# Kernel optimization log

Measured on AMD Instinct MI355X. Metric: run time of the kernel, lower is better.

The kernel has to match this reference:

```python
import jax, jax.numpy as jnp
import numpy as np

VOCAB = 32000
EMBED = 8      # == d_k == n_qubits (forced by the module's reshapes)
NQ = 8
DEPTH = 2
NBLOCKS = 6
FFN = 8        # == n_qubits (forced)
NCLASSES = 10
B, S = 32, 1024
LN_EPS = 1e-5

_H = np.array([[1.0, 1.0], [1.0, -1.0]], np.complex64) / np.sqrt(2.0).astype(np.float32)


def _posenc(seq, dim):
    pos = np.arange(seq, dtype=np.float32)[:, None]
    div = np.exp(np.arange(0, dim, 2, dtype=np.float32) * (-np.log(10000.0) / dim))
    pe = np.zeros((seq, dim), np.float32)
    pe[:, 0::2] = np.sin(pos * div)
    pe[:, 1::2] = np.cos(pos * div)
    return jnp.asarray(pe)


def _quantum_head(x, depth=DEPTH):
    """Batched statevector simulation of the QNode. x: (N, NQ) angles -> (N, NQ) Z expvals."""
    N, n = x.shape
    c = jnp.cos(0.5 * x).astype(jnp.complex64)
    s = jnp.sin(0.5 * x).astype(jnp.complex64)
    amp = jnp.stack([c, -1j * s], axis=-1)  # (N, n, 2): RX(theta)|0>
    state = amp[:, 0]  # product state built wire by wire -> (N, 2, ..., 2)
    for i in range(1, n):
        state = state[..., None] * amp[:, i].reshape((N,) + (1,) * (state.ndim - 1) + (2,))
    Hm = jnp.asarray(_H)
    for _ in range(depth):
        for i in range(n - 1):  # CNOT(i, i+1): flip target slice where control==1
            s0 = jnp.take(state, 0, axis=i + 1)
            s1 = jnp.flip(jnp.take(state, 1, axis=i + 1), axis=i + 1)
            state = jnp.stack([s0, s1], axis=i + 1)
        state = jnp.einsum('...i,ij->...j', state, Hm)  # Hadamard on last wire
    probs = state.real ** 2 + state.imag ** 2  # (N, 2, ..., 2)
    zs = []
    for i in range(n):
        axes = tuple(a for a in range(1, n + 1) if a != i + 1)
        m = probs.sum(axis=axes)  # (N, 2) marginal of wire i
        zs.append(m[:, 0] - m[:, 1])
    return jnp.stack(zs, axis=-1)


def _ln(x, g, b):
    m = x.mean(axis=-1, keepdims=True)
    v = ((x - m) ** 2).mean(axis=-1, keepdims=True)
    return g * (x - m) / jnp.sqrt(v + LN_EPS) + b


def _forward(tokens, emb, ln1_g, ln1_b, ln2_g, ln2_b, attn_w, attn_b,
             ffn_w1, ffn_b1, ffn_w2, ffn_b2, cls_w, cls_b):
    Bt, St = tokens.shape
    E = emb.shape[1]
    x = emb[tokens] + _posenc(St, E)[None]  # (B, S, E)
    scale = float(1.0 / np.sqrt(E))
    for l in range(NBLOCKS):
        # quantum attention (num_heads == 1, d_k == E)
        qkv = _quantum_head(x.reshape(-1, E)).reshape(Bt, St, E)
        scores = jnp.einsum('bqd,bkd->bqk', qkv, qkv) * scale
        attn = jax.nn.softmax(scores, axis=-1)
        out = jnp.einsum('bqk,bkd->bqd', attn, qkv)
        attn_out = out @ attn_w[l] + attn_b[l]
        x = _ln(x + attn_out, ln1_g[l], ln1_b[l])
        # quantum FFN
        h = x @ ffn_w1[l] + ffn_b1[l]  # (B, S, FFN)
        qf = _quantum_head(h.reshape(-1, FFN)).reshape(Bt, St, FFN)
        ffn_out = qf @ ffn_w2[l] + ffn_b2[l]
        x = _ln(x + ffn_out, ln2_g[l], ln2_b[l])
    pooled = x.mean(axis=1)  # (B, E)
    return pooled @ cls_w + cls_b  # (B, NCLASSES)


def setup_inputs() -> dict:
    key = jax.random.key(0)
    ks = jax.random.split(key, 8)
    f32 = jnp.float32
    L, E, F = NBLOCKS, EMBED, FFN
    return {
        'tokens': jax.random.randint(ks[0], (B, S), 0, VOCAB),
        'emb': jax.random.normal(ks[1], (VOCAB, E), f32) * 0.1,
        'ln1_g': jnp.ones((L, E), f32), 'ln1_b': jnp.zeros((L, E), f32),
        'ln2_g': jnp.ones((L, E), f32), 'ln2_b': jnp.zeros((L, E), f32),
        'attn_w': jax.random.normal(ks[2], (L, E, E), f32) * 0.3,
        'attn_b': jnp.zeros((L, E), f32),
        'ffn_w1': jax.random.normal(ks[3], (L, E, F), f32) * 0.3,
        'ffn_b1': jnp.zeros((L, F), f32),
        'ffn_w2': jax.random.normal(ks[4], (L, F, E), f32) * 0.3,
        'ffn_b2': jnp.zeros((L, E), f32),
        'cls_w': jax.random.normal(ks[5], (E, NCLASSES), f32) * 0.3,
        'cls_b': jnp.zeros((NCLASSES,), f32),
    }


def reference(tokens, emb, ln1_g, ln1_b, ln2_g, ln2_b, attn_w, attn_b,
              ffn_w1, ffn_b1, ffn_w2, ffn_b2, cls_w, cls_b):
    return _forward(tokens, emb, ln1_g, ln1_b, ln2_g, ln2_b, attn_w, attn_b,
                    ffn_w1, ffn_b1, ffn_w2, ffn_b2, cls_w, cls_b)
```

## Files before the change

kernel.cpp:

```cpp
#include <hip/hip_runtime.h>
#include <math.h>

#define EMB 8
#define SEQ 1024
#define NBATCH 32
#define NROWS (NBATCH * SEQ)
#define LNEPS 1e-5f
#define F2(l, b, c) (((l) * 32 + (b)) * 32 + (c))

typedef __attribute__((ext_vector_type(4))) unsigned u32x4;
typedef __attribute__((ext_vector_type(8))) _Float16 f16x8;
typedef __attribute__((ext_vector_type(16))) float f32x16;

union FragU { unsigned u[4]; f16x8 s; };

__device__ __forceinline__ unsigned pkrtz(float a, float b) {
    unsigned r;
    asm("v_cvt_pkrtz_f16_f32 %0, %1, %2" : "=v"(r) : "v"(a), "v"(b));
    return r;
}
__device__ __forceinline__ unsigned pk_mul_f16(unsigned a, unsigned b) {
    unsigned r;
    asm("v_pk_mul_f16 %0, %1, %2" : "=v"(r) : "v"(a), "v"(b));
    return r;
}
__device__ __forceinline__ float hw_exp2(float x) {
    return __builtin_amdgcn_exp2f(x);
}

__device__ __forceinline__ void llc_load_2rows(const unsigned short* p,
                                               u32x4* d0, u32x4* d1) {
    asm volatile(
        "global_load_dwordx4 %0, %[a], off sc0 sc1\n\t"
        "global_load_dwordx4 %1, %[a], off offset:16 sc0 sc1\n\t"
        "s_waitcnt vmcnt(0)"
        : "=&v"(*d0), "=&v"(*d1) : [a] "v"(p) : "memory");
}
__device__ __forceinline__ void llc_store_row16(unsigned short* p, u32x4 v) {
    asm volatile("global_store_dwordx4 %[a], %[x], off sc0 sc1"
                 :: [a] "v"(p), [x] "v"(v) : "memory");
}
__device__ __forceinline__ void sys_store(float* p, float v) {
    asm volatile("global_store_dword %0, %1, off sc0 sc1" :: "v"(p), "v"(v) : "memory");
}
__device__ __forceinline__ float sys_load(const float* p) {
    float r;
    asm volatile("global_load_dword %0, %1, off sc0 sc1\n\ts_waitcnt vmcnt(0)"
                 : "=v"(r) : "v"(p) : "memory");
    return r;
}
__device__ __forceinline__ unsigned sys_load_u32(const unsigned* p) {
    unsigned r;
    asm volatile("global_load_dword %0, %1, off sc0 sc1\n\ts_waitcnt vmcnt(0)"
                 : "=v"(r) : "v"(p) : "memory");
    return r;
}
__device__ __forceinline__ void sys_store_u32(unsigned* p, unsigned v) {
    asm volatile("global_store_dword %0, %1, off sc0 sc1" :: "v"(p), "v"(v) : "memory");
}

__device__ __forceinline__ void qhead(const float xv[8], float z[8]) {
    float c[8];
#pragma unroll
    for (int j = 0; j < 8; ++j) c[j] = __cosf(xv[j]);
    float e0 = c[0];
    float o1 = c[1];
    float e2 = e0 * c[2];
    float o3 = o1 * c[3];
    float e4 = e2 * c[4];
    float o5 = o3 * c[5];
    float e6 = e4 * c[6];
    z[0] = e0; z[1] = o1; z[2] = e2; z[3] = o3;
    z[4] = e4; z[5] = o5; z[6] = e6;
    z[7] = e6 * o5 * c[7];
}

__device__ __forceinline__ void embed_row(const int* __restrict__ tokens,
                                          const float* __restrict__ emb,
                                          long grow, int srow, float xv[8]) {
    int tok = tokens[grow];
    const float* e = emb + (long)tok * EMB;
    float p = (float)srow;
    xv[0] = e[0] + sinf(p);
    xv[1] = e[1] + cosf(p);
    xv[2] = e[2] + sinf(p * 0.1f);
    xv[3] = e[3] + cosf(p * 0.1f);
    xv[4] = e[4] + sinf(p * 0.01f);
    xv[5] = e[5] + cosf(p * 0.01f);
    xv[6] = e[6] + sinf(p * 0.001f);
    xv[7] = e[7] + cosf(p * 0.001f);
}

__global__ __launch_bounds__(1024) void zero_flags(unsigned* __restrict__ f) {
    for (int i = threadIdx.x; i < 6656; i += 1024) f[i] = 0u;
}

__global__ __launch_bounds__(512, 4) void qt_fused(
    const int* __restrict__ tokens, const float* __restrict__ emb,
    const float* __restrict__ attn_w, const float* __restrict__ attn_b,
    const float* __restrict__ ln1_g, const float* __restrict__ ln1_b,
    const float* __restrict__ ffn_w1, const float* __restrict__ ffn_b1,
    const float* __restrict__ ffn_w2, const float* __restrict__ ffn_b2,
    const float* __restrict__ ln2_g, const float* __restrict__ ln2_b,
    const float* __restrict__ cls_w, const float* __restrict__ cls_b,
    unsigned short* __restrict__ qkv0, unsigned short* __restrict__ qkv1,
    unsigned* __restrict__ flags, unsigned* __restrict__ pcnt,
    float* __restrict__ partial, float* __restrict__ out)
{
    __shared__ __align__(16) uint2 KbP[2][1024];
    __shared__ __align__(16) unsigned short VtH[8][1032];
    __shared__ float Olds[8][32][9];
    __shared__ float x_lds[2][32][8];
    __shared__ int isL[2];

    const int bid = blockIdx.x;
    const int group = bid & 15;
    const int chunk = bid >> 4;
    const int tid = threadIdx.x;

    const int w = tid >> 6;
    const int lane = tid & 63;
    const int ln = lane & 31;
    const int h = lane >> 5;
    const int qbase = chunk * 32;
    const unsigned B2PK = pkrtz(0.51006972f, 0.51006972f);

    for (int l = 0; l < 6; ++l) {
        const unsigned short* qr = (l & 1) ? qkv1 : qkv0;
        unsigned short* qw = (l & 1) ? qkv0 : qkv1;
        for (int ph = 0; ph < 2; ++ph) {
            const int bb = group * 2 + ph;
            {
                u32x4 d0, d1;
                if (l == 0) {
                    float e0[8], e1[8], z0[8], z1[8];
                    embed_row(tokens, emb, (long)bb * SEQ + 2 * tid, 2 * tid, e0);
                    embed_row(tokens, emb, (long)bb * SEQ + 2 * tid + 1, 2 * tid + 1, e1);
                    if ((tid >> 4) == chunk) {
                        const int lr = 2 * tid - chunk * 32;
#pragma unroll
                        for (int j = 0; j < 8; ++j) {
                            x_lds[ph][lr][j] = e0[j];
                            x_lds[ph][lr + 1][j] = e1[j];
                        }
                    }
                    qhead(e0, z0); qhead(e1, z1);
                    d0[0] = pkrtz(z0[0], z0[1]); d0[1] = pkrtz(z0[2], z0[3]);
                    d0[2] = pkrtz(z0[4], z0[5]); d0[3] = pkrtz(z0[6], z0[7]);
                    d1[0] = pkrtz(z1[0], z1[1]); d1[1] = pkrtz(z1[2], z1[3]);
                    d1[2] = pkrtz(z1[4], z1[5]); d1[3] = pkrtz(z1[6], z1[7]);
                } else {
                    const unsigned* fp = &flags[F2(l, bb, tid >> 4)];
                    while (sys_load_u32(fp) == 0u) __builtin_amdgcn_s_sleep(1);
                    llc_load_2rows(qr + ((long)bb * SEQ + 2 * tid) * 8, &d0, &d1);
                }
                u32x4 kp0, kp1;
                kp0[0] = d0[0]; kp0[1] = d0[1]; kp0[2] = d1[0]; kp0[3] = d1[1];
                kp1[0] = d0[2]; kp1[1] = d0[3]; kp1[2] = d1[2]; kp1[3] = d1[3];
                *(u32x4*)&KbP[0][2 * tid] = kp0;
                *(u32x4*)&KbP[1][2 * tid] = kp1;
#pragma unroll
                for (int c = 0; c < 8; ++c) {
                    unsigned wa = d0[c >> 1], wb = d1[c >> 1];
                    unsigned v = (c & 1) ? ((wa >> 16) | (wb & 0xFFFF0000u))
                                         : ((wa & 0xFFFFu) | (wb << 16));
                    *(unsigned*)&VtH[c][2 * tid] = v;
                }
            }
            __syncthreads();

            FragU qfB;
            {
                uint2 qh = KbP[h][qbase + ln];
                unsigned qx = pk_mul_f16(qh.x, B2PK);
                unsigned qy = pk_mul_f16(qh.y, B2PK);
                qfB.u[0] = qx; qfB.u[1] = qy; qfB.u[2] = qx; qfB.u[3] = qy;
            }
            f32x16 zc;
#pragma unroll
            for (int i = 0; i < 16; ++i) zc[i] = 0.f;
            f32x16 accA = zc, accB = zc;

#pragma unroll
            for (int t = 0; t < 4; ++t) {
                const int kbase = (w * 4 + t) * 32;
                FragU kfA;
                {
                    uint2 kh = KbP[h][kbase + ln];
                    kfA.u[0] = kh.x; kfA.u[1] = kh.y; kfA.u[2] = 0; kfA.u[3] = 0;
                }
                f32x16 s = __builtin_amdgcn_mfma_f32_32x32x16_f16(kfA.s, qfB.s, zc, 0, 0, 0);
                float p[16];
#pragma unroll
                for (int g = 0; g < 16; ++g) p[g] = hw_exp2(s[g]);

                FragU a1, a2;
#pragma unroll
                for (int vi = 0; vi < 4; ++vi) {
                    a1.u[vi] = pkrtz(p[2 * vi], p[2 * vi + 1]);
                    a2.u[vi] = pkrtz(p[8 + 2 * vi], p[8 + 2 * vi + 1]);
                }
                FragU v1h, v2h;
                if (ln < 8) {
                    const unsigned* q0 = (const unsigned*)&VtH[ln][kbase + 4 * h];
                    const unsigned* q1 = (const unsigned*)&VtH[ln][kbase + 8 + 4 * h];
                    const unsigned* q2 = (const unsigned*)&VtH[ln][kbase + 16 + 4 * h];
                    const unsigned* q3 = (const unsigned*)&VtH[ln][kbase + 24 + 4 * h];
                    v1h.u[0] = q0[0]; v1h.u[1] = q0[1]; v1h.u[2] = q1[0]; v1h.u[3] = q1[1];
                    v2h.u[0] = q2[0]; v2h.u[1] = q2[1]; v2h.u[2] = q3[0]; v2h.u[3] = q3[1];
                } else if (ln == 8) {
#pragma unroll
                    for (int i = 0; i < 4; ++i) { v1h.u[i] = 0x3C003C00u; v2h.u[i] = 0x3C003C00u; }
                } else {
#pragma unroll
                    for (int i = 0; i < 4; ++i) { v1h.u[i] = 0; v2h.u[i] = 0; }
                }
                accA = __builtin_amdgcn_mfma_f32_32x32x16_f16(a1.s, v1h.s, accA, 0, 0, 0);
                accB = __builtin_amdgcn_mfma_f32_32x32x16_f16(a2.s, v2h.s, accB, 0, 0, 0);
            }

            if (ln <= 8) {
#pragma unroll
                for (int g = 0; g < 16; ++g)
                    Olds[w][(g & 3) + 8 * (g >> 2) + 4 * h][ln] = accA[g] + accB[g];
            }
            __syncthreads();

            if ((tid >> 6) == ph && lane < 32) {
                const int r = lane;
                float o[9];
#pragma unroll
                for (int c = 0; c < 9; ++c) {
                    float s01 = Olds[0][r][c] + Olds[1][r][c];
                    float s23 = Olds[2][r][c] + Olds[3][r][c];
                    float s45 = Olds[4][r][c] + Olds[5][r][c];
                    float s67 = Olds[6][r][c] + Olds[7][r][c];
                    o[c] = (s01 + s23) + (s45 + s67);
                }
                float inv = 1.0f / o[8];
                float outv[8];
#pragma unroll
                for (int c = 0; c < 8; ++c) outv[c] = o[c] * inv;

                const float* W  = attn_w + l * 64; const float* Wb  = attn_b + l * 8;
                const float* g1 = ln1_g + l * 8;   const float* b1v = ln1_b + l * 8;
                const float* W1 = ffn_w1 + l * 64; const float* c1  = ffn_b1 + l * 8;
                const float* W2 = ffn_w2 + l * 64; const float* c2  = ffn_b2 + l * 8;
                const float* g2 = ln2_g + l * 8;   const float* b2v = ln2_b + l * 8;

                float xv[8];
#pragma unroll
                for (int j = 0; j < 8; ++j) xv[j] = x_lds[ph][r][j];

                float y[8]; float m = 0.f;
#pragma unroll
                for (int j = 0; j < 8; ++j) {
                    float vv = Wb[j];
#pragma unroll
                    for (int i = 0; i < 8; ++i) vv += outv[i] * W[i * 8 + j];
                    y[j] = xv[j] + vv;
                    m += y[j];
                }
                m *= 0.125f;
                float var = 0.f;
#pragma unroll
                for (int j = 0; j < 8; ++j) { float dd = y[j] - m; var += dd * dd; }
                var *= 0.125f;
                float rsg = rsqrtf(var + LNEPS);
                float xn[8];
#pragma unroll
                for (int j = 0; j < 8; ++j) xn[j] = g1[j] * (y[j] - m) * rsg + b1v[j];

                float hh[8];
#pragma unroll
                for (int j = 0; j < 8; ++j) {
                    float vv = c1[j];
#pragma unroll
                    for (int i = 0; i < 8; ++i) vv += xn[i] * W1[i * 8 + j];
                    hh[j] = vv;
                }
                float qff[8]; qhead(hh, qff);
                float m2 = 0.f;
#pragma unroll
                for (int j = 0; j < 8; ++j) {
                    float vv = c2[j];
#pragma unroll
                    for (int i = 0; i < 8; ++i) vv += qff[i] * W2[i * 8 + j];
                    y[j] = xn[j] + vv;
                    m2 += y[j];
                }
                m2 *= 0.125f;
                float var2 = 0.f;
#pragma unroll
                for (int j = 0; j < 8; ++j) { float dd = y[j] - m2; var2 += dd * dd; }
                var2 *= 0.125f;
                float rs2 = rsqrtf(var2 + LNEPS);
#pragma unroll
                for (int j = 0; j < 8; ++j) {
                    float xo = g2[j] * (y[j] - m2) * rs2 + b2v[j];
                    x_lds[ph][r][j] = xo;
                    xv[j] = xo;
                }

                if (l < 5) {
                    float z[8]; qhead(xv, z);
                    u32x4 pz;
                    pz[0] = pkrtz(z[0], z[1]); pz[1] = pkrtz(z[2], z[3]);
                    pz[2] = pkrtz(z[4], z[5]); pz[3] = pkrtz(z[6], z[7]);
                    llc_store_row16(qw + ((long)bb * SEQ + chunk * 32 + r) * 8, pz);
                    asm volatile("s_waitcnt vmcnt(0)" ::: "memory");
                    if (r == 0) sys_store_u32(&flags[F2(l + 1, bb, chunk)], 1u);
                }
            }
        }
    }

    if ((tid >> 6) < 2) {
        const int ph = tid >> 6;
        const int r = tid & 63;
        const int bb = group * 2 + ph;
        float a[8];
#pragma unroll
        for (int j = 0; j < 8; ++j) {
            a[j] = (r < 32) ? x_lds[ph][r][j] : 0.f;
#pragma unroll
            for (int off = 1; off <= 32; off <<= 1) a[j] += __shfl_xor(a[j], off);
        }
        if (r < 8) sys_store(&partial[(bb * 32 + chunk) * 8 + r], a[r]);
    }
    asm volatile("s_waitcnt vmcnt(0)" ::: "memory");
    __syncthreads();
    if (tid == 0) {
        unsigned r = __hip_atomic_fetch_add(&pcnt[(group * 2) * 16], 1u,
                                            __ATOMIC_RELAXED, __HIP_MEMORY_SCOPE_AGENT);
        isL[0] = (r == 31u);
    }
    if (tid == 64) {
        unsigned r = __hip_atomic_fetch_add(&pcnt[(group * 2 + 1) * 16], 1u,
                                            __ATOMIC_RELAXED, __HIP_MEMORY_SCOPE_AGENT);
        isL[1] = (r == 31u);
    }
    __syncthreads();
    if ((tid >> 6) < 2) {
        const int ph = tid >> 6;
        if (isL[ph]) {
            const int bb = group * 2 + ph;
            const int lr = tid & 63;
            int g = lr >> 3, j = lr & 7;
            float s = sys_load(&partial[(bb * 32 + g) * 8 + j])
                    + sys_load(&partial[(bb * 32 + g + 8) * 8 + j])
                    + sys_load(&partial[(bb * 32 + g + 16) * 8 + j])
                    + sys_load(&partial[(bb * 32 + g + 24) * 8 + j]);
            s += __shfl_xor(s, 8); s += __shfl_xor(s, 16); s += __shfl_xor(s, 32);
            float poolj = s * (1.0f / 1024.0f);
            int c = lr < 10 ? lr : 9;
            float o = cls_b[c];
#pragma unroll
            for (int j2 = 0; j2 < 8; ++j2)
                o += __shfl(poolj, j2) * cls_w[j2 * 10 + c];
            if (lr < 10) out[bb * 10 + lr] = o;
        }
    }
}

extern "C" void kernel_launch(void* const* d_in, const int* in_sizes, int n_in,
                              void* d_out, int out_size, void* d_ws, size_t ws_size,
                              hipStream_t stream) {
    const int*   tokens = (const int*)d_in[0];
    const float* emb    = (const float*)d_in[1];
    const float* ln1_g  = (const float*)d_in[2];
    const float* ln1_b  = (const float*)d_in[3];
    const float* ln2_g  = (const float*)d_in[4];
    const float* ln2_b  = (const float*)d_in[5];
    const float* attn_w = (const float*)d_in[6];
    const float* attn_b = (const float*)d_in[7];
    const float* ffn_w1 = (const float*)d_in[8];
    const float* ffn_b1 = (const float*)d_in[9];
    const float* ffn_w2 = (const float*)d_in[10];
    const float* ffn_b2 = (const float*)d_in[11];
    const float* cls_w  = (const float*)d_in[12];
    const float* cls_b  = (const float*)d_in[13];

    unsigned*       flags   = (unsigned*)d_ws;
    unsigned*       pcnt    = flags + 6144;
    float*          partial = (float*)(pcnt + 512);
    unsigned short* qkv0    = (unsigned short*)(partial + 8192);
    unsigned short* qkv1    = qkv0 + (long)NROWS * 8;
    float*          outp    = (float*)d_out;

    zero_flags<<<1, 1024, 0, stream>>>(flags);
    qt_fused<<<512, 512, 0, stream>>>(
        tokens, emb, attn_w, attn_b, ln1_g, ln1_b,
        ffn_w1, ffn_b1, ffn_w2, ffn_b2, ln2_g, ln2_b,
        cls_w, cls_b, qkv0, qkv1, flags, pcnt, partial, outp);
}
```

Measured before the change: 89.07 us.

## Halve grid to 256 blocks, each handling 64 query rows across two tiles

Each block now processes 64 query rows per batch (two 32-row tiles split across wave groups) instead of 32, so the grid shrinks from 512 to 256 blocks. This halves the redundant per-block work of loading and staging the full K/V sequence into shared memory and the number of cross-block flag waits. The trade is more attention work per wave (8 key tiles instead of 4) and fewer resident blocks, which may lengthen the serial per-layer critical path. Flags, partials and the final reduction are resized to match.

```diff
diff --git a/kernel.cpp b/kernel.cpp
--- a/kernel.cpp
+++ b/kernel.cpp
@@ -6,7 +6,7 @@
 #define NBATCH 32
 #define NROWS (NBATCH * SEQ)
 #define LNEPS 1e-5f
-#define F2(l, b, c) (((l) * 32 + (b)) * 32 + (c))
+#define F(l, b, c) (((l) * 32 + (b)) * 16 + (c))
 
 typedef __attribute__((ext_vector_type(4))) unsigned u32x4;
 typedef __attribute__((ext_vector_type(8))) _Float16 f16x8;
@@ -92,10 +92,10 @@
 }
 
 __global__ __launch_bounds__(1024) void zero_flags(unsigned* __restrict__ f) {
-    for (int i = threadIdx.x; i < 6656; i += 1024) f[i] = 0u;
-}
-
-__global__ __launch_bounds__(512, 4) void qt_fused(
+    for (int i = threadIdx.x; i < 3584; i += 1024) f[i] = 0u;
+}
+
+__global__ __launch_bounds__(512, 2) void qt_fused(
     const int* __restrict__ tokens, const float* __restrict__ emb,
     const float* __restrict__ attn_w, const float* __restrict__ attn_b,
     const float* __restrict__ ln1_g, const float* __restrict__ ln1_b,
@@ -110,7 +110,7 @@
     __shared__ __align__(16) uint2 KbP[2][1024];
     __shared__ __align__(16) unsigned short VtH[8][1032];
     __shared__ float Olds[8][32][9];
-    __shared__ float x_lds[2][32][8];
+    __shared__ float x_lds[2][64][8];
     __shared__ int isL[2];
 
     const int bid = blockIdx.x;
@@ -122,7 +122,9 @@
     const int lane = tid & 63;
     const int ln = lane & 31;
     const int h = lane >> 5;
-    const int qbase = chunk * 32;
+    const int qtile = w >> 2;
+    const int qu = w & 3;
+    const int r0 = tid * 2;
     const unsigned B2PK = pkrtz(0.51006972f, 0.51006972f);
 
     for (int l = 0; l < 6; ++l) {
@@ -134,10 +136,10 @@
                 u32x4 d0, d1;
                 if (l == 0) {
                     float e0[8], e1[8], z0[8], z1[8];
-                    embed_row(tokens, emb, (long)bb * SEQ + 2 * tid, 2 * tid, e0);
-                    embed_row(tokens, emb, (long)bb * SEQ + 2 * tid + 1, 2 * tid + 1, e1);
-                    if ((tid >> 4) == chunk) {
-                        const int lr = 2 * tid - chunk * 32;
+                    embed_row(tokens, emb, (long)bb * SEQ + r0, r0, e0);
+                    embed_row(tokens, emb, (long)bb * SEQ + r0 + 1, r0 + 1, e1);
+                    if ((r0 >> 6) == chunk) {
+                        const int lr = r0 - chunk * 64;
 #pragma unroll
                         for (int j = 0; j < 8; ++j) {
                             x_lds[ph][lr][j] = e0[j];
@@ -150,25 +152,26 @@
                     d1[0] = pkrtz(z1[0], z1[1]); d1[1] = pkrtz(z1[2], z1[3]);
                     d1[2] = pkrtz(z1[4], z1[5]); d1[3] = pkrtz(z1[6], z1[7]);
                 } else {
-                    const unsigned* fp = &flags[F2(l, bb, tid >> 4)];
+                    const unsigned* fp = &flags[F(l, bb, r0 >> 6)];
                     while (sys_load_u32(fp) == 0u) __builtin_amdgcn_s_sleep(1);
-                    llc_load_2rows(qr + ((long)bb * SEQ + 2 * tid) * 8, &d0, &d1);
+                    llc_load_2rows(qr + ((long)bb * SEQ + r0) * 8, &d0, &d1);
                 }
                 u32x4 kp0, kp1;
                 kp0[0] = d0[0]; kp0[1] = d0[1]; kp0[2] = d1[0]; kp0[3] = d1[1];
                 kp1[0] = d0[2]; kp1[1] = d0[3]; kp1[2] = d1[2]; kp1[3] = d1[3];
-                *(u32x4*)&KbP[0][2 * tid] = kp0;
-                *(u32x4*)&KbP[1][2 * tid] = kp1;
+                *(u32x4*)&KbP[0][r0] = kp0;
+                *(u32x4*)&KbP[1][r0] = kp1;
 #pragma unroll
                 for (int c = 0; c < 8; ++c) {
                     unsigned wa = d0[c >> 1], wb = d1[c >> 1];
                     unsigned v = (c & 1) ? ((wa >> 16) | (wb & 0xFFFF0000u))
                                          : ((wa & 0xFFFFu) | (wb << 16));
-                    *(unsigned*)&VtH[c][2 * tid] = v;
+                    *(unsigned*)&VtH[c][r0] = v;
                 }
             }
             __syncthreads();
 
+            const int qbase = chunk * 64 + qtile * 32;
             FragU qfB;
             {
                 uint2 qh = KbP[h][qbase + ln];
@@ -180,10 +183,16 @@
 #pragma unroll
             for (int i = 0; i < 16; ++i) zc[i] = 0.f;
             f32x16 accA = zc, accB = zc;
-
-#pragma unroll
-            for (int t = 0; t < 4; ++t) {
-                const int kbase = (w * 4 + t) * 32;
+            FragU v1c, v2c;
+            {
+                const unsigned fill = (ln == 8) ? 0x3C003C00u : 0u;
+#pragma unroll
+                for (int i = 0; i < 4; ++i) { v1c.u[i] = fill; v2c.u[i] = fill; }
+            }
+
+#pragma unroll 2
+            for (int t = 0; t < 8; ++t) {
+                const int kbase = ((qu << 3) | t) << 5;
                 FragU kfA;
                 {
                     uint2 kh = KbP[h][kbase + ln];
@@ -200,7 +209,7 @@
                     a1.u[vi] = pkrtz(p[2 * vi], p[2 * vi + 1]);
                     a2.u[vi] = pkrtz(p[8 + 2 * vi], p[8 + 2 * vi + 1]);
                 }
-                FragU v1h, v2h;
+                FragU v1h = v1c, v2h = v2c;
                 if (ln < 8) {
                     const unsigned* q0 = (const unsigned*)&VtH[ln][kbase + 4 * h];
                     const unsigned* q1 = (const unsigned*)&VtH[ln][kbase + 8 + 4 * h];
@@ -208,12 +217,6 @@
                     const unsigned* q3 = (const unsigned*)&VtH[ln][kbase + 24 + 4 * h];
                     v1h.u[0] = q0[0]; v1h.u[1] = q0[1]; v1h.u[2] = q1[0]; v1h.u[3] = q1[1];
                     v2h.u[0] = q2[0]; v2h.u[1] = q2[1]; v2h.u[2] = q3[0]; v2h.u[3] = q3[1];
-                } else if (ln == 8) {
-#pragma unroll
-                    for (int i = 0; i < 4; ++i) { v1h.u[i] = 0x3C003C00u; v2h.u[i] = 0x3C003C00u; }
-                } else {
-#pragma unroll
-                    for (int i = 0; i < 4; ++i) { v1h.u[i] = 0; v2h.u[i] = 0; }
                 }
                 accA = __builtin_amdgcn_mfma_f32_32x32x16_f16(a1.s, v1h.s, accA, 0, 0, 0);
                 accB = __builtin_amdgcn_mfma_f32_32x32x16_f16(a2.s, v2h.s, accB, 0, 0, 0);
@@ -226,17 +229,15 @@
             }
             __syncthreads();
 
-            if ((tid >> 6) == ph && lane < 32) {
-                const int r = lane;
+            if ((tid >> 6) == ph) {
+                const int r = tid & 63;
+                const int rr = r & 31;
+                const int w0 = (r >> 5) * 4;
                 float o[9];
 #pragma unroll
-                for (int c = 0; c < 9; ++c) {
-                    float s01 = Olds[0][r][c] + Olds[1][r][c];
-                    float s23 = Olds[2][r][c] + Olds[3][r][c];
-                    float s45 = Olds[4][r][c] + Olds[5][r][c];
-                    float s67 = Olds[6][r][c] + Olds[7][r][c];
-                    o[c] = (s01 + s23) + (s45 + s67);
-                }
+                for (int c = 0; c < 9; ++c)
+                    o[c] = (Olds[w0][rr][c] + Olds[w0 + 1][rr][c])
+                         + (Olds[w0 + 2][rr][c] + Olds[w0 + 3][rr][c]);
                 float inv = 1.0f / o[8];
                 float outv[8];
 #pragma unroll
@@ -307,9 +308,9 @@
                     u32x4 pz;
                     pz[0] = pkrtz(z[0], z[1]); pz[1] = pkrtz(z[2], z[3]);
                     pz[2] = pkrtz(z[4], z[5]); pz[3] = pkrtz(z[6], z[7]);
-                    llc_store_row16(qw + ((long)bb * SEQ + chunk * 32 + r) * 8, pz);
+                    llc_store_row16(qw + ((long)bb * SEQ + chunk * 64 + r) * 8, pz);
                     asm volatile("s_waitcnt vmcnt(0)" ::: "memory");
-                    if (r == 0) sys_store_u32(&flags[F2(l + 1, bb, chunk)], 1u);
+                    if (r == 0) sys_store_u32(&flags[F(l + 1, bb, chunk)], 1u);
                 }
             }
         }
@@ -322,23 +323,23 @@
         float a[8];
 #pragma unroll
         for (int j = 0; j < 8; ++j) {
-            a[j] = (r < 32) ? x_lds[ph][r][j] : 0.f;
+            a[j] = x_lds[ph][r][j];
 #pragma unroll
             for (int off = 1; off <= 32; off <<= 1) a[j] += __shfl_xor(a[j], off);
         }
-        if (r < 8) sys_store(&partial[(bb * 32 + chunk) * 8 + r], a[r]);
+        if (r < 8) sys_store(&partial[(bb * 16 + chunk) * 8 + r], a[r]);
     }
     asm volatile("s_waitcnt vmcnt(0)" ::: "memory");
     __syncthreads();
     if (tid == 0) {
         unsigned r = __hip_atomic_fetch_add(&pcnt[(group * 2) * 16], 1u,
                                             __ATOMIC_RELAXED, __HIP_MEMORY_SCOPE_AGENT);
-        isL[0] = (r == 31u);
+        isL[0] = (r == 15u);
     }
     if (tid == 64) {
         unsigned r = __hip_atomic_fetch_add(&pcnt[(group * 2 + 1) * 16], 1u,
                                             __ATOMIC_RELAXED, __HIP_MEMORY_SCOPE_AGENT);
-        isL[1] = (r == 31u);
+        isL[1] = (r == 15u);
     }
     __syncthreads();
     if ((tid >> 6) < 2) {
@@ -347,10 +348,8 @@
             const int bb = group * 2 + ph;
             const int lr = tid & 63;
             int g = lr >> 3, j = lr & 7;
-            float s = sys_load(&partial[(bb * 32 + g) * 8 + j])
-                    + sys_load(&partial[(bb * 32 + g + 8) * 8 + j])
-                    + sys_load(&partial[(bb * 32 + g + 16) * 8 + j])
-                    + sys_load(&partial[(bb * 32 + g + 24) * 8 + j]);
+            float s = sys_load(&partial[(bb * 16 + g) * 8 + j])
+                    + sys_load(&partial[(bb * 16 + g + 8) * 8 + j]);
             s += __shfl_xor(s, 8); s += __shfl_xor(s, 16); s += __shfl_xor(s, 32);
             float poolj = s * (1.0f / 1024.0f);
             int c = lr < 10 ? lr : 9;
@@ -382,14 +381,14 @@
     const float* cls_b  = (const float*)d_in[13];
 
     unsigned*       flags   = (unsigned*)d_ws;
-    unsigned*       pcnt    = flags + 6144;
+    unsigned*       pcnt    = flags + 3072;
     float*          partial = (float*)(pcnt + 512);
-    unsigned short* qkv0    = (unsigned short*)(partial + 8192);
+    unsigned short* qkv0    = (unsigned short*)(partial + 4096);
     unsigned short* qkv1    = qkv0 + (long)NROWS * 8;
     float*          outp    = (float*)d_out;
 
     zero_flags<<<1, 1024, 0, stream>>>(flags);
-    qt_fused<<<512, 512, 0, stream>>>(
+    qt_fused<<<256, 512, 0, stream>>>(
         tokens, emb, attn_w, attn_b, ln1_g, ln1_b,
         ffn_w1, ffn_b1, ffn_w2, ffn_b2, ln2_g, ln2_b,
         cls_w, cls_b, qkv0, qkv1, flags, pcnt, partial, outp);
```

Result: faster. 75.41 us (median of 2 runs) (-15.3%).
